# Kernel tuning notes

Hardware: AMD Instinct MI355X
Metric: run time of the kernel (lower is better)

The kernel has to match this reference:

```python
import jax, jax.numpy as jnp
import numpy as np

EPS = 1e-5

def _batchnorm(x, gamma, beta):
    # BatchNorm1d in training mode: stats over the point (N) dimension, biased var
    mean = x.mean(axis=0)
    var = ((x - mean) ** 2).mean(axis=0)
    return (x - mean) * jax.lax.rsqrt(var + EPS) * gamma + beta

def setup_inputs() -> dict:
    key = jax.random.key(0)
    ks = jax.random.split(key, 6)
    N, C_in, K, B = 262144, 3, 64, 16
    return {
        "feats": jax.random.normal(ks[0], (N, C_in), dtype=jnp.float32),
        "batch_idx": jax.random.randint(ks[1], (N,), 0, B, dtype=jnp.int32),
        "W1": jax.random.normal(ks[2], (128, C_in), dtype=jnp.float32) * 0.1,
        "gamma1": jnp.ones((128,), jnp.float32),
        "beta1": jnp.zeros((128,), jnp.float32),
        "W2": jax.random.normal(ks[3], (64, 256), dtype=jnp.float32) * 0.05,
        "gamma2": jnp.ones((64,), jnp.float32),
        "beta2": jnp.zeros((64,), jnp.float32),
        "W3": jax.random.normal(ks[4], (K, 64), dtype=jnp.float32) * 0.1,
        "b3": jnp.zeros((K,), jnp.float32),
        "num_batches": B,
    }

def reference(feats, batch_idx, W1, gamma1, beta1, W2, gamma2, beta2, W3, b3, num_batches):
    # conv1 (1x1 conv == linear, no bias) + bn1
    x = _batchnorm(feats @ W1.T, gamma1, beta1)          # [N,128]
    # per-batch global max pooling, broadcast back to points
    seg_max = jax.ops.segment_max(x, batch_idx, num_segments=num_batches)  # [B,128]
    x = jnp.concatenate([x, seg_max[batch_idx]], axis=1)  # [N,256]
    # conv2 + bn2 + relu
    x = jax.nn.relu(_batchnorm(x @ W2.T, gamma2, beta2))  # [N,64]
    # conv3 (with bias)
    return x @ W3.T + b3                                   # [N,k]
```

## Files before the change

kernel.cpp:

```cpp
#include <hip/hip_runtime.h>
#include <hip/hip_bf16.h>

#define EPS 1e-5f
#define NPTS 262144
#define NB 16

typedef __attribute__((ext_vector_type(8))) short bf16x8;
typedef __attribute__((ext_vector_type(4))) float f32x4;

#define WS_E    0
#define WS_T    192
#define WS_W3   1216
#define WS_MAXF 3264
#define WS_PMOM 5312
#define WS_SCRM 6480
#define WS_SMAX 43856

__device__ inline float decodeu(unsigned u){
  unsigned bits = (u & 0x80000000u) ? (u ^ 0x80000000u) : ~u;
  return __uint_as_float(bits);
}
__device__ inline unsigned f2bf(float f){
  unsigned u = __float_as_uint(f);
  return (u + 0x7FFFu + ((u>>16)&1u)) >> 16;
}
__device__ inline unsigned pack2bf(float lo, float hi){
  return (f2bf(hi)<<16) | (f2bf(lo) & 0xFFFFu);
}
__device__ inline unsigned ordu(float v){
  unsigned bits = __float_as_uint(v);
  return bits ^ (unsigned)(((int)bits>>31) | (int)0x80000000);
}

__global__ __launch_bounds__(512) void kAC(const float* __restrict__ feats,
                                           const int* __restrict__ bidx,
                                           const float* __restrict__ W1,
                                           const float* __restrict__ g1,
                                           float* __restrict__ wsf) {
  __shared__ unsigned lmax[NB*128];
  __shared__ __align__(16) float4 sfeat[512];
  __shared__ float hist[4][NB*4];
  __shared__ float red[8*9];
  __shared__ unsigned cnt[NB], base[NB];
  int tid = threadIdx.x;
  int lane = tid&63, wv = tid>>6;
  for (int i=tid;i<NB*128;i+=512) lmax[i]=0u;
  if (tid < 4*NB*4) ((float*)hist)[tid]=0.f;
  if (tid < NB) cnt[tid]=0u;
  __syncthreads();
  int p = blockIdx.x*512 + tid;
  float f0=feats[3*p], f1=feats[3*p+1], f2=feats[3*p+2];
  int b = bidx[p];
  int hrep = wv >> 1;
  atomicAdd(&hist[hrep][b*4+0],f0);
  atomicAdd(&hist[hrep][b*4+1],f1);
  atomicAdd(&hist[hrep][b*4+2],f2);
  atomicAdd(&hist[hrep][b*4+3],1.0f);
  unsigned pos = atomicAdd(&cnt[b], 1u);
  { float acc[9]={f0,f1,f2,f0*f0,f0*f1,f0*f2,f1*f1,f1*f2,f2*f2};
    #pragma unroll
    for (int k=0;k<9;k++){
      float v=acc[k];
      v+=__shfl_down(v,32); v+=__shfl_down(v,16); v+=__shfl_down(v,8);
      v+=__shfl_down(v,4);  v+=__shfl_down(v,2);  v+=__shfl_down(v,1);
      if (lane==0) red[wv*9+k]=v;
    }
  }
  __syncthreads();
  if (tid==0){
    unsigned s=0;
    #pragma unroll
    for (int q=0;q<NB;q++){ base[q]=s; s+=cnt[q]; }
  }
  __syncthreads();
  sfeat[base[b]+pos] = make_float4(f0,f1,f2,__int_as_float(b));
  __syncthreads();
  int c0 = lane, c1 = lane+64;
  float sg0 = (g1[c0]>=0.f)?1.f:-1.f;
  float sg1 = (g1[c1]>=0.f)?1.f:-1.f;
  float w00=W1[3*c0]*sg0, w01=W1[3*c0+1]*sg0, w02=W1[3*c0+2]*sg0;
  float w10=W1[3*c1]*sg1, w11=W1[3*c1+1]*sg1, w12=W1[3*c1+2]*sg1;
  const float4* sp = &sfeat[wv*64];
  int bcur = -1; float mm0=0.f, mm1=0.f;
  #pragma unroll 8
  for (int k=0;k<64;k++){
    float4 f = sp[k];
    float v0 = fmaf(f.z,w02,fmaf(f.y,w01,f.x*w00));
    float v1 = fmaf(f.z,w12,fmaf(f.y,w11,f.x*w10));
    int b2 = __builtin_amdgcn_readfirstlane(__float_as_int(f.w));
    if (b2 != bcur){
      if (bcur >= 0){
        atomicMax(&lmax[bcur*128+c0], ordu(mm0));
        atomicMax(&lmax[bcur*128+c1], ordu(mm1));
      }
      bcur = b2; mm0 = v0; mm1 = v1;
    } else {
      mm0 = fmaxf(mm0,v0); mm1 = fmaxf(mm1,v1);
    }
  }
  atomicMax(&lmax[bcur*128+c0], ordu(mm0));
  atomicMax(&lmax[bcur*128+c1], ordu(mm1));
  __syncthreads();
  float* scrM = wsf + WS_SCRM + blockIdx.x*73;
  if (tid<9){
    float s=0;
    #pragma unroll
    for (int q=0;q<8;q++) s += red[q*9+tid];
    scrM[tid]=s;
  }
  if (tid>=64 && tid<128){
    int i = tid-64;
    scrM[9+i] = hist[0][i]+hist[1][i]+hist[2][i]+hist[3][i];
  }
  unsigned* spo = (unsigned*)wsf + WS_SMAX + (size_t)blockIdx.x*2048;
  for (int i=tid;i<2048;i+=512) spo[i]=lmax[i];
}

__global__ __launch_bounds__(512) void kMx(const float* __restrict__ W3,
                                           float* __restrict__ wsf){
  __shared__ unsigned red[32][16];
  __shared__ float mred[2][73];
  int tid = threadIdx.x, blk = blockIdx.x;
  int g = tid >> 4;
  int e = blk*16 + (tid & 15);
  const unsigned* smax = (const unsigned*)wsf + WS_SMAX;
  unsigned m = 0;
  #pragma unroll 8
  for (int k=g*16; k<g*16+16; k++){
    unsigned t = smax[(size_t)k*2048 + e];
    m = t>m ? t : m;
  }
  red[g][tid&15] = m;
  if (blk < 16 && tid < 146){
    int h = (tid >= 73) ? 1 : 0, mm = tid - 73*h;
    float s = 0; const float* sm0 = wsf + WS_SCRM;
    int k0 = blk*32 + h*16;
    #pragma unroll 4
    for (int k=k0; k<k0+16; k++) s += sm0[k*73 + mm];
    mred[h][mm] = s;
  }
  if (blk >= 32 && blk < 34){
    int q = (blk-32)*512 + tid;
    float4 v = ((const float4*)W3)[q];
    unsigned* w3u = (unsigned*)wsf + WS_W3;
    w3u[2*q]   = pack2bf(v.x, v.y);
    w3u[2*q+1] = pack2bf(v.z, v.w);
  }
  __syncthreads();
  if (tid < 16){
    unsigned u = red[0][tid];
    #pragma unroll
    for (int q=1;q<32;q++){ unsigned t=red[q][tid]; u = t>u?t:u; }
    ((unsigned*)wsf)[WS_MAXF + blk*16 + tid] = u;
  }
  if (blk < 16 && tid < 73)
    wsf[WS_PMOM + blk*73 + tid] = mred[0][tid] + mred[1][tid];
}

__global__ __launch_bounds__(128) void kB2(const float* __restrict__ W1,
    const float* __restrict__ g1, const float* __restrict__ b1,
    const float* __restrict__ W2, const float* __restrict__ g2,
    const float* __restrict__ b2, float* __restrict__ wsf){
  __shared__ float spm[16*73];
  __shared__ float smom[80];
  __shared__ float dred[2][20];
  __shared__ float sfin[20];
  __shared__ float pY[16], pYY[16], hbs[16];
  __shared__ float s2t2[2];
  int tid = threadIdx.x, c = blockIdx.x;
  int lane = tid & 63, wv = tid >> 6;
  for (int i=tid;i<16*73;i+=128) spm[i] = wsf[WS_PMOM + i];
  int j = tid;
  float w2f = W2[c*256 + j];
  float w2b = W2[c*256 + 128 + j];
  float w10 = W1[3*j], w11 = W1[3*j+1], w12 = W1[3*j+2];
  float g1j = g1[j], b1j = b1[j];
  unsigned um[16];
  { const unsigned* mf = (const unsigned*)wsf + WS_MAXF;
    #pragma unroll
    for (int b=0;b<16;b++) um[b] = mf[b*128 + j];
  }
  __syncthreads();
  if (tid < 73){
    float s = 0;
    #pragma unroll
    for (int g=0; g<16; g++) s += spm[g*73 + tid];
    smom[tid] = s;
  }
  __syncthreads();
  const float invN = 1.0f/NPTS;
  float mean = (w10*smom[0]+w11*smom[1]+w12*smom[2])*invN;
  float ex2 = (w10*w10*smom[3]+w11*w11*smom[6]+w12*w12*smom[8]
             + 2.f*(w10*w11*smom[4]+w10*w12*smom[5]+w11*w12*smom[7]))*invN;
  float var = ex2 - mean*mean;
  float sc = g1j*rsqrtf(var+EPS);
  float sh = b1j - mean*sc;
  float asc = fabsf(sc);
  float p[20];
  p[0] = w2f*(sc*w10); p[1] = w2f*(sc*w11); p[2] = w2f*(sc*w12); p[3] = w2f*sh;
  #pragma unroll
  for (int b=0;b<16;b++) p[4+b] = w2b * fmaf(asc, decodeu(um[b]), sh);
  #pragma unroll
  for (int k=0;k<20;k++){
    float v = p[k];
    v+=__shfl_down(v,32); v+=__shfl_down(v,16); v+=__shfl_down(v,8);
    v+=__shfl_down(v,4);  v+=__shfl_down(v,2);  v+=__shfl_down(v,1);
    if (lane==0) dred[wv][k] = v;
  }
  __syncthreads();
  if (tid < 20) sfin[tid] = dred[0][tid] + dred[1][tid];
  __syncthreads();
  if (tid < 16){
    int b = tid;
    float e0=sfin[0],e1=sfin[1],e2=sfin[2],gc=sfin[3];
    float nb = smom[9+b*4+3];
    float hb = gc + sfin[4+b];
    float eS1b = e0*smom[9+b*4]+e1*smom[9+b*4+1]+e2*smom[9+b*4+2];
    hbs[b]=hb; pY[b]=nb*hb; pYY[b]=2.f*hb*eS1b+nb*hb*hb;
  }
  __syncthreads();
  if (tid == 0){
    float e0=sfin[0],e1=sfin[1],e2=sfin[2];
    float sumY = e0*smom[0]+e1*smom[1]+e2*smom[2];
    float sumYY = e0*e0*smom[3]+e1*e1*smom[6]+e2*e2*smom[8]
               + 2.f*(e0*e1*smom[4]+e0*e2*smom[5]+e1*e2*smom[7]);
    #pragma unroll
    for (int b=0;b<16;b++){ sumY += pY[b]; sumYY += pYY[b]; }
    float mean2 = sumY*invN;
    float var2 = sumYY*invN - mean2*mean2;
    float s2 = g2[c]*rsqrtf(var2+EPS);
    float t2 = b2[c] - mean2*s2;
    wsf[WS_E + c]      = e0*s2;
    wsf[WS_E + 64 + c] = e1*s2;
    wsf[WS_E + 128 + c]= e2*s2;
    s2t2[0]=s2; s2t2[1]=t2;
  }
  __syncthreads();
  if (tid < 16) wsf[WS_T + tid*64 + c] = hbs[tid]*s2t2[0] + s2t2[1];
}

__global__ __launch_bounds__(256, 4) void kF(const float* __restrict__ feats,
                                             const int* __restrict__ bidx,
                                             const float* __restrict__ wsf,
                                             const float* __restrict__ b3,
                                             float* __restrict__ out) {
  __shared__ __align__(16) unsigned char SB[39936];
  unsigned* zbuf = (unsigned*)SB;
  float* fbuf = (float*)SB;
  float* Tl = (float*)(SB + 34816);
  float* sEg = (float*)(SB + 39168);
  int tid = threadIdx.x;
  for (int i=tid;i<NB*64;i+=256) Tl[(i>>6)*68 + (i&63)] = wsf[WS_T + i];
  if (tid < 192) sEg[tid] = wsf[WS_E + tid];
  int lane = tid & 63, wv = tid >> 6;
  int col = lane & 15, kgrp = lane >> 4;
  const ushort* w3b = (const ushort*)((const unsigned*)wsf + WS_W3);
  bf16x8 bfr[4][2];
  #pragma unroll
  for (int n=0;n<4;n++)
    #pragma unroll
    for (int kk=0;kk<2;kk++)
      bfr[n][kk] = *(const bf16x8*)(w3b + (n*16+col)*64 + kk*32 + kgrp*8);
  float bias[4];
  #pragma unroll
  for (int n=0;n<4;n++) bias[n] = b3[n*16+col];
  const f32x4* e04 = (const f32x4*)(sEg);
  const f32x4* e14 = (const f32x4*)(sEg + 64);
  const f32x4* e24 = (const f32x4*)(sEg + 128);
  __syncthreads();
  #pragma unroll 1
  for (int tile=0; tile<2; ++tile){
    int tb_idx = blockIdx.x*2 + tile;
    int p0 = (tb_idx*4 + wv)*64;
    int p = p0 + lane;
    float f0 = feats[3*p], f1 = feats[3*p+1], f2 = feats[3*p+2];
    int b = bidx[p];
    const f32x4* tb4 = (const f32x4*)&Tl[b*68];
    unsigned rowbase = (unsigned)(wv*64+lane)*32;
    unsigned sw = (lane&7)<<2;
    #pragma unroll
    for (int j=0;j<8;j++){
      unsigned w[4];
      #pragma unroll
      for (int h=0;h<2;h++){
        int cq = j*2 + h;
        f32x4 e0 = e04[cq], e1 = e14[cq], e2 = e24[cq], tp = tb4[cq];
        float y0 = fmaf(e0[0],f0, fmaf(e1[0],f1, fmaf(e2[0],f2, tp[0])));
        float y1 = fmaf(e0[1],f0, fmaf(e1[1],f1, fmaf(e2[1],f2, tp[1])));
        float y2 = fmaf(e0[2],f0, fmaf(e1[2],f1, fmaf(e2[2],f2, tp[2])));
        float y3 = fmaf(e0[3],f0, fmaf(e1[3],f1, fmaf(e2[3],f2, tp[3])));
        w[h*2]   = pack2bf(fmaxf(y0,0.f), fmaxf(y1,0.f));
        w[h*2+1] = pack2bf(fmaxf(y2,0.f), fmaxf(y3,0.f));
      }
      uint4 ch; ch.x=w[0]; ch.y=w[1]; ch.z=w[2]; ch.w=w[3];
      *(uint4*)&zbuf[rowbase + (((unsigned)(j*4)) ^ sw)] = ch;
    }
    __syncthreads();
    bf16x8 af[4][2];
    #pragma unroll
    for (int m=0;m<4;m++){
      int row = m*16 + col;
      unsigned rb = (unsigned)(wv*64+row)*32;
      unsigned sw2 = (unsigned)(row&7)<<2;
      #pragma unroll
      for (int kk=0;kk<2;kk++){
        unsigned off = ((unsigned)(kk*16 + kgrp*4)) ^ sw2;
        af[m][kk] = *(const bf16x8*)&zbuf[rb + off];
      }
    }
    __syncthreads();
    #pragma unroll
    for (int half=0; half<2; half++){
      f32x4 acc[2][4];
      #pragma unroll
      for (int mi=0;mi<2;mi++)
        #pragma unroll
        for (int n=0;n<4;n++)
          acc[mi][n] = (f32x4){0.f,0.f,0.f,0.f};
      #pragma unroll
      for (int kk=0;kk<2;kk++)
        #pragma unroll
        for (int mi=0;mi<2;mi++)
          #pragma unroll
          for (int n=0;n<4;n++)
            acc[mi][n] = __builtin_amdgcn_mfma_f32_16x16x32_bf16(af[half*2+mi][kk], bfr[n][kk], acc[mi][n], 0,0,0);
      #pragma unroll
      for (int mi=0;mi<2;mi++){
        #pragma unroll
        for (int n=0;n<4;n++){
          #pragma unroll
          for (int r=0;r<4;r++)
            fbuf[wv*2176 + (mi*16 + kgrp*4 + r)*68 + n*16 + col] = acc[mi][n][r] + bias[n];
        }
      }
      __syncthreads();
      #pragma unroll
      for (int it=0; it<8; it++){
        int idx = it*256 + tid;
        int gr = idx >> 4;
        int c4 = (idx & 15) * 4;
        f32x4 v = *(const f32x4*)&fbuf[(gr>>5)*2176 + (gr&31)*68 + c4];
        int orow = tb_idx*256 + (gr>>5)*64 + half*32 + (gr&31);
        __builtin_nontemporal_store(v, (f32x4*)&out[(size_t)orow*64 + c4]);
      }
      __syncthreads();
    }
  }
}

extern "C" void kernel_launch(void* const* d_in, const int* in_sizes, int n_in,
                              void* d_out, int out_size, void* d_ws, size_t ws_size,
                              hipStream_t stream) {
  const float* feats = (const float*)d_in[0];
  const int*   bidx  = (const int*)d_in[1];
  const float* W1 = (const float*)d_in[2];
  const float* g1 = (const float*)d_in[3];
  const float* b1 = (const float*)d_in[4];
  const float* W2 = (const float*)d_in[5];
  const float* g2 = (const float*)d_in[6];
  const float* b2 = (const float*)d_in[7];
  const float* W3 = (const float*)d_in[8];
  const float* b3 = (const float*)d_in[9];
  float* wsf = (float*)d_ws;
  float* out = (float*)d_out;
  kAC<<<512, 512, 0, stream>>>(feats, bidx, W1, g1, wsf);
  kMx<<<128, 512, 0, stream>>>(W3, wsf);
  kB2<<<64, 128, 0, stream>>>(W1, g1, b1, W2, g2, b2, wsf);
  kF<<<512, 256, 0, stream>>>(feats, bidx, wsf, b3, out);
}
```

Measured before the change: 54.38 us.

## Make final kernel wave-private, drop block barriers, launch one tile per block

The final fused kernel now gives each wave its own shared-memory region for the staged bf16 activations and the fp32 output tile. This replaces block-wide __syncthreads with per-wave lgkmcnt waits and scheduling barriers. The two-tile loop per block is removed and the grid doubles to 1024 blocks, and the output staging drops its row padding, which shrinks shared memory. This trades barrier stalls for possible LDS bank conflicts on the unpadded output buffer and relies on waves only touching their own region.

```diff
diff --git a/kernel.cpp b/kernel.cpp
--- a/kernel.cpp
+++ b/kernel.cpp
@@ -244,11 +244,10 @@
                                              const float* __restrict__ wsf,
                                              const float* __restrict__ b3,
                                              float* __restrict__ out) {
-  __shared__ __align__(16) unsigned char SB[39936];
+  __shared__ __align__(16) unsigned char SB[37888];
   unsigned* zbuf = (unsigned*)SB;
-  float* fbuf = (float*)SB;
-  float* Tl = (float*)(SB + 34816);
-  float* sEg = (float*)(SB + 39168);
+  float* Tl = (float*)(SB + 32768);
+  float* sEg = (float*)(SB + 37120);
   int tid = threadIdx.x;
   for (int i=tid;i<NB*64;i+=256) Tl[(i>>6)*68 + (i&63)] = wsf[WS_T + i];
   if (tid < 192) sEg[tid] = wsf[WS_E + tid];
@@ -268,83 +267,84 @@
   const f32x4* e14 = (const f32x4*)(sEg + 64);
   const f32x4* e24 = (const f32x4*)(sEg + 128);
   __syncthreads();
-  #pragma unroll 1
-  for (int tile=0; tile<2; ++tile){
-    int tb_idx = blockIdx.x*2 + tile;
-    int p0 = (tb_idx*4 + wv)*64;
-    int p = p0 + lane;
-    float f0 = feats[3*p], f1 = feats[3*p+1], f2 = feats[3*p+2];
-    int b = bidx[p];
-    const f32x4* tb4 = (const f32x4*)&Tl[b*68];
-    unsigned rowbase = (unsigned)(wv*64+lane)*32;
-    unsigned sw = (lane&7)<<2;
-    #pragma unroll
-    for (int j=0;j<8;j++){
-      unsigned w[4];
+  int p0 = (blockIdx.x*4 + wv)*64;
+  int p = p0 + lane;
+  float f0 = feats[3*p], f1 = feats[3*p+1], f2 = feats[3*p+2];
+  int b = bidx[p];
+  const f32x4* tb4 = (const f32x4*)&Tl[b*68];
+  unsigned rowbase = (unsigned)(wv*64+lane)*32;
+  unsigned sw = (lane&7)<<2;
+  #pragma unroll
+  for (int j=0;j<8;j++){
+    unsigned w[4];
+    #pragma unroll
+    for (int h=0;h<2;h++){
+      int cq = j*2 + h;
+      f32x4 e0 = e04[cq], e1 = e14[cq], e2 = e24[cq], tp = tb4[cq];
+      float y0 = fmaf(e0[0],f0, fmaf(e1[0],f1, fmaf(e2[0],f2, tp[0])));
+      float y1 = fmaf(e0[1],f0, fmaf(e1[1],f1, fmaf(e2[1],f2, tp[1])));
+      float y2 = fmaf(e0[2],f0, fmaf(e1[2],f1, fmaf(e2[2],f2, tp[2])));
+      float y3 = fmaf(e0[3],f0, fmaf(e1[3],f1, fmaf(e2[3],f2, tp[3])));
+      w[h*2]   = pack2bf(fmaxf(y0,0.f), fmaxf(y1,0.f));
+      w[h*2+1] = pack2bf(fmaxf(y2,0.f), fmaxf(y3,0.f));
+    }
+    uint4 ch; ch.x=w[0]; ch.y=w[1]; ch.z=w[2]; ch.w=w[3];
+    *(uint4*)&zbuf[rowbase + (((unsigned)(j*4)) ^ sw)] = ch;
+  }
+  asm volatile("s_waitcnt lgkmcnt(0)" ::: "memory");
+  __builtin_amdgcn_sched_barrier(0);
+  bf16x8 af[4][2];
+  #pragma unroll
+  for (int m=0;m<4;m++){
+    int row = m*16 + col;
+    unsigned rb = (unsigned)(wv*64+row)*32;
+    unsigned sw2 = (unsigned)(row&7)<<2;
+    #pragma unroll
+    for (int kk=0;kk<2;kk++){
+      unsigned off = ((unsigned)(kk*16 + kgrp*4)) ^ sw2;
+      af[m][kk] = *(const bf16x8*)&zbuf[rb + off];
+    }
+  }
+  asm volatile("s_waitcnt lgkmcnt(0)" ::: "memory");
+  __builtin_amdgcn_sched_barrier(0);
+  float* fwave = (float*)(SB + wv*8192);
+  #pragma unroll
+  for (int half=0; half<2; half++){
+    f32x4 acc[2][4];
+    #pragma unroll
+    for (int mi=0;mi<2;mi++)
       #pragma unroll
-      for (int h=0;h<2;h++){
-        int cq = j*2 + h;
-        f32x4 e0 = e04[cq], e1 = e14[cq], e2 = e24[cq], tp = tb4[cq];
-        float y0 = fmaf(e0[0],f0, fmaf(e1[0],f1, fmaf(e2[0],f2, tp[0])));
-        float y1 = fmaf(e0[1],f0, fmaf(e1[1],f1, fmaf(e2[1],f2, tp[1])));
-        float y2 = fmaf(e0[2],f0, fmaf(e1[2],f1, fmaf(e2[2],f2, tp[2])));
-        float y3 = fmaf(e0[3],f0, fmaf(e1[3],f1, fmaf(e2[3],f2, tp[3])));
-        w[h*2]   = pack2bf(fmaxf(y0,0.f), fmaxf(y1,0.f));
-        w[h*2+1] = pack2bf(fmaxf(y2,0.f), fmaxf(y3,0.f));
-      }
-      uint4 ch; ch.x=w[0]; ch.y=w[1]; ch.z=w[2]; ch.w=w[3];
-      *(uint4*)&zbuf[rowbase + (((unsigned)(j*4)) ^ sw)] = ch;
-    }
-    __syncthreads();
-    bf16x8 af[4][2];
-    #pragma unroll
-    for (int m=0;m<4;m++){
-      int row = m*16 + col;
-      unsigned rb = (unsigned)(wv*64+row)*32;
-      unsigned sw2 = (unsigned)(row&7)<<2;
-      #pragma unroll
-      for (int kk=0;kk<2;kk++){
-        unsigned off = ((unsigned)(kk*16 + kgrp*4)) ^ sw2;
-        af[m][kk] = *(const bf16x8*)&zbuf[rb + off];
-      }
-    }
-    __syncthreads();
-    #pragma unroll
-    for (int half=0; half<2; half++){
-      f32x4 acc[2][4];
+      for (int n=0;n<4;n++)
+        acc[mi][n] = (f32x4){0.f,0.f,0.f,0.f};
+    #pragma unroll
+    for (int kk=0;kk<2;kk++)
       #pragma unroll
       for (int mi=0;mi<2;mi++)
         #pragma unroll
         for (int n=0;n<4;n++)
-          acc[mi][n] = (f32x4){0.f,0.f,0.f,0.f};
+          acc[mi][n] = __builtin_amdgcn_mfma_f32_16x16x32_bf16(af[half*2+mi][kk], bfr[n][kk], acc[mi][n], 0,0,0);
+    #pragma unroll
+    for (int mi=0;mi<2;mi++){
       #pragma unroll
-      for (int kk=0;kk<2;kk++)
+      for (int n=0;n<4;n++){
         #pragma unroll
-        for (int mi=0;mi<2;mi++)
-          #pragma unroll
-          for (int n=0;n<4;n++)
-            acc[mi][n] = __builtin_amdgcn_mfma_f32_16x16x32_bf16(af[half*2+mi][kk], bfr[n][kk], acc[mi][n], 0,0,0);
-      #pragma unroll
-      for (int mi=0;mi<2;mi++){
-        #pragma unroll
-        for (int n=0;n<4;n++){
-          #pragma unroll
-          for (int r=0;r<4;r++)
-            fbuf[wv*2176 + (mi*16 + kgrp*4 + r)*68 + n*16 + col] = acc[mi][n][r] + bias[n];
-        }
+        for (int r=0;r<4;r++)
+          fwave[(mi*16 + kgrp*4 + r)*64 + n*16 + col] = acc[mi][n][r] + bias[n];
       }
-      __syncthreads();
-      #pragma unroll
-      for (int it=0; it<8; it++){
-        int idx = it*256 + tid;
-        int gr = idx >> 4;
-        int c4 = (idx & 15) * 4;
-        f32x4 v = *(const f32x4*)&fbuf[(gr>>5)*2176 + (gr&31)*68 + c4];
-        int orow = tb_idx*256 + (gr>>5)*64 + half*32 + (gr&31);
-        __builtin_nontemporal_store(v, (f32x4*)&out[(size_t)orow*64 + c4]);
-      }
-      __syncthreads();
-    }
+    }
+    asm volatile("s_waitcnt lgkmcnt(0)" ::: "memory");
+    __builtin_amdgcn_sched_barrier(0);
+    #pragma unroll
+    for (int it=0; it<8; it++){
+      int idx = it*64 + lane;
+      int r = idx >> 4;
+      int c4 = (idx & 15) * 4;
+      f32x4 v = *(const f32x4*)&fwave[r*64 + c4];
+      int orow = p0 + half*32 + r;
+      __builtin_nontemporal_store(v, (f32x4*)&out[(size_t)orow*64 + c4]);
+    }
+    asm volatile("s_waitcnt lgkmcnt(0)" ::: "memory");
+    __builtin_amdgcn_sched_barrier(0);
   }
 }
 
@@ -366,5 +366,5 @@
   kAC<<<512, 512, 0, stream>>>(feats, bidx, W1, g1, wsf);
   kMx<<<128, 512, 0, stream>>>(W3, wsf);
   kB2<<<64, 128, 0, stream>>>(W1, g1, b1, W2, g2, b2, wsf);
-  kF<<<512, 256, 0, stream>>>(feats, bidx, wsf, b3, out);
-}
+  kF<<<1024, 256, 0, stream>>>(feats, bidx, wsf, b3, out);
+}
```

After: 53.62 us. No clear change (-1.4%).
